# Performance work log

Hardware: AMD Instinct MI355X
Metric: run time of the kernel (lower is better)

Reference implementation:

```python
import jax, jax.numpy as jnp
import numpy as np

IMG_SIZE = 416
NUM_CLASSES = 80
IGNORE_THR = 0.5
EPS = 1e-12
# raw YOLOv3 anchors per feature map, scaled by that level's stride (32,16,8)
ANCHORS = np.array([[[116,90],[156,198],[373,326]],
                    [[30,61],[62,45],[59,119]],
                    [[10,13],[16,30],[33,23]]], dtype=np.float32)
SCALED_ANCHORS = ANCHORS / np.array([32.0,16.0,8.0], dtype=np.float32)[:,None,None]  # [M=3,K=3,2]


def _get_target(targets, total_anchors, fsizes, last_num):
    # Vectorized translation of YOLO3Loss.get_target (including its 3*gi*gj indexing scheme).
    B, N, _ = targets.shape
    A = total_anchors
    sa = jnp.asarray(SCALED_ANCHORS)
    M, K, _ = SCALED_ANCHORS.shape
    fs = jnp.asarray(fsizes, dtype=targets.dtype)        # [M]
    ln = jnp.asarray(last_num, dtype=jnp.int32)          # [M] anchor offsets per level

    valid = jnp.sum(targets, axis=-1) != 0               # [B,N] skip all-zero rows
    cls_idx = targets[..., 0].astype(jnp.int32)          # int(target[b,n,0])
    gx = targets[..., 1:2] * fs                          # [B,N,M]
    gy = targets[..., 2:3] * fs
    gw = targets[..., 3:4] * fs
    gh = targets[..., 4:5] * fs
    gi = jnp.floor(gx).astype(jnp.int32)
    gj = jnp.floor(gy).astype(jnp.int32)

    # IoU of (0,0,gw,gh) gt boxes vs (0,0,aw,ah) anchor shapes -> [B,N,M,K]
    aw, ah = sa[..., 0], sa[..., 1]                      # [M,K]
    inter = jnp.minimum(gw[..., None], aw) * jnp.minimum(gh[..., None], ah)
    union = gw[..., None] * gh[..., None] + aw * ah - inter
    iou = inter / (union + 1e-16)

    # noobj_mask: zero every anchor whose IoU exceeds the ignore threshold
    cell = ln + K * gi * gj                              # [B,N,M]  (last_num[m] + 3*gi*gj)
    idx_no = cell[..., None] + jnp.arange(K)             # [B,N,M,K]
    hit = valid[..., None, None] & (iou > IGNORE_THR)
    safe_no = jnp.where(hit, idx_no, A)                  # route inactive scatters to dummy slot A
    bb = jnp.arange(B)[:, None, None, None]
    noobj = jnp.ones((B, A + 1), targets.dtype).at[bb, safe_no].set(0.0)[:, :A]

    # best anchor over all feature maps
    best_iou_m = jnp.max(iou, -1)                        # [B,N,M]
    best_a_m = jnp.argmax(iou, -1)
    bf = jnp.argmax(best_iou_m, -1)                      # [B,N] best feature map
    take = lambda arr: jnp.take_along_axis(arr, bf[..., None], axis=-1)[..., 0]
    best_a = take(best_a_m)
    gi_b, gj_b = take(gi), take(gj)
    idx_best = ln[bf] + K * gi_b * gj_b + best_a         # [B,N]
    tconf_v = jnp.max(best_iou_m, -1)

    safe = jnp.where(valid, idx_best, A)
    b2 = jnp.arange(B)[:, None]
    def scat(vals):
        return jnp.zeros((B, A + 1), targets.dtype).at[b2, safe].set(vals)[:, :A]
    mask = scat(jnp.ones_like(tconf_v))
    tx = scat(targets[..., 1] * IMG_SIZE)
    ty = scat(targets[..., 2] * IMG_SIZE)
    tw = scat(targets[..., 3] * IMG_SIZE)
    th = scat(targets[..., 4] * IMG_SIZE)
    wwh = scat(2.0 - targets[..., 3] * targets[..., 4])
    tconf = scat(tconf_v)
    tcls = jnp.zeros((B, A + 1, NUM_CLASSES), targets.dtype).at[b2, safe, cls_idx].set(1.0)[:, :A]
    return mask, noobj, tx, ty, tw, th, wwh, tconf, tcls


def _bce(p, t):
    p = jnp.clip(p, EPS, 1.0 - EPS)
    return jnp.mean(-(t * jnp.log(p) + (1.0 - t) * jnp.log(1.0 - p)))


def yolo_loss(prediction, targets, stride):
    B, A, _ = prediction.shape
    M, K, _ = SCALED_ANCHORS.shape
    fsizes = [int(IMG_SIZE / stride * (2 ** i)) for i in range(M)]
    last_num = [0]
    for i in range(M - 1):
        last_num.append(last_num[i] + K * fsizes[i] ** 2)
    mask, noobj, tx, ty, tw, th, wwh, tconf, tcls = _get_target(targets, A, fsizes, last_num)

    x, y = prediction[..., 0], prediction[..., 1]
    w, h = prediction[..., 2], prediction[..., 3]
    conf = prediction[..., 4]
    pcls = prediction[..., 5:]

    mse = lambda a, b: jnp.mean((a - b) ** 2)
    loss_x = mse(x * mask * wwh, tx * wwh)
    loss_y = mse(y * mask * wwh, ty * wwh)
    loss_w = mse(w * mask * wwh, tw * wwh)
    loss_h = mse(h * mask * wwh, th * wwh)
    loss_conf = _bce(conf * mask, tconf) + 0.5 * _bce(conf * noobj, jnp.zeros_like(conf))

    # BCE over boolean-indexed positive rows == mask-weighted mean over all rows
    p = jnp.clip(pcls, EPS, 1.0 - EPS)
    elem = -(tcls * jnp.log(p) + (1.0 - tcls) * jnp.log(1.0 - p))
    npos = jnp.sum(mask)
    loss_cls = jnp.sum(elem * mask[..., None]) / (npos * NUM_CLASSES)
    return loss_x + loss_y + loss_w + loss_h + loss_conf + loss_cls


def setup_inputs() -> dict:
    key = jax.random.key(0)
    k1, k2, k3, k4 = jax.random.split(key, 4)
    B, N, A, C = 64, 50, 10647, NUM_CLASSES
    cls = jax.random.randint(k1, (B, N, 1), 0, C).astype(jnp.float32)
    xy = jax.random.uniform(k2, (B, N, 2), minval=0.05, maxval=0.95)
    wh = jax.random.uniform(k3, (B, N, 2), minval=0.02, maxval=0.4)
    targets = jnp.concatenate([cls, xy, wh], axis=-1)
    # last 10 target slots per image are padding (all zeros -> skipped)
    targets = targets * (jnp.arange(N) < 40).astype(jnp.float32)[None, :, None]
    prediction = jax.random.uniform(k4, (B, A, 5 + C), minval=1e-4, maxval=1.0 - 1e-4)
    return {"prediction": prediction, "targets": targets, "stride": 32}


def reference(prediction, targets, stride):
    return yolo_loss(prediction, targets, stride)
```

## Files before the change

kernel.cpp:

```cpp
#include <hip/hip_runtime.h>
#include <math.h>

#define A_TOT   10647
#define BATCH   64
#define NTGT    50
#define NC      80
#define MAXREC  64
#define MAXHIT  512
#define TOT_CELLS (BATCH * A_TOT)
#define NB4     666
#define CHUNK   1024

struct Rec {
    int cell;
    float tx, ty, tw, th, wwh, tconf;
    unsigned c0, c1, c2;
};

__global__ __launch_bounds__(64) void phaseA(const float* __restrict__ tgt,
                                             int* __restrict__ counts,
                                             Rec* __restrict__ recs,
                                             int* __restrict__ hitcnt,
                                             int* __restrict__ hitlist,
                                             double* __restrict__ sums) {
    __shared__ int   s_valid[64];
    __shared__ int   s_idx[64];
    __shared__ float s_tx[64], s_ty[64], s_tw[64], s_th[64], s_wwh[64], s_tc[64];
    __shared__ int   s_cls[64];
    __shared__ Rec   s_rec[NTGT];
    __shared__ int   s_cnt;
    __shared__ unsigned s_bm[336];
    __shared__ int   s_hits[MAXHIT];
    __shared__ int   s_hc;

    const int b = blockIdx.x;
    const int n = threadIdx.x;

    if (b == 0 && n == 0) {
        sums[0] = 0.0; sums[1] = 0.0; sums[2] = 0.0;
    }

    for (int i = n; i < 336; i += 64) s_bm[i] = 0u;
    if (n == 0) s_hc = 0;
    __syncthreads();

    const float fs[3] = {13.f, 26.f, 52.f};
    const int   ln[3] = {0, 507, 2535};
    const float aw[3][3] = {{3.625f, 4.875f, 11.65625f},
                            {1.875f, 3.875f, 3.6875f},
                            {1.25f,  2.0f,   4.125f}};
    const float ah[3][3] = {{2.8125f, 6.1875f, 10.1875f},
                            {3.8125f, 2.8125f, 7.4375f},
                            {1.625f,  3.75f,   2.875f}};

    int valid = 0;
    if (n < NTGT) {
        const float* t = tgt + (size_t)(b * NTGT + n) * 5;
        float t0 = t[0], t1 = t[1], t2 = t[2], t3 = t[3], t4 = t[4];
        valid = ((t0 + t1 + t2 + t3 + t4) != 0.0f);
        if (valid) {
            float best_m_iou = -1.f;
            int bf = 0, best_a = 0, gi_b = 0, gj_b = 0;
            for (int m = 0; m < 3; m++) {
                float gw = t3 * fs[m], gh = t4 * fs[m];
                int gi = (int)floorf(t1 * fs[m]);
                int gj = (int)floorf(t2 * fs[m]);
                float bi = -1.f; int bk = 0;
                for (int k = 0; k < 3; k++) {
                    float in_ = fminf(gw, aw[m][k]) * fminf(gh, ah[m][k]);
                    float un  = gw * gh + aw[m][k] * ah[m][k] - in_;
                    float iou = in_ / (un + 1e-16f);
                    if (iou > bi) { bi = iou; bk = k; }
                    if (iou > 0.5f) {
                        int cell = ln[m] + 3 * gi * gj + k;
                        unsigned bit = 1u << (cell & 31);
                        unsigned old = atomicOr(&s_bm[cell >> 5], bit);
                        if (!(old & bit)) {
                            int pos = atomicAdd(&s_hc, 1);
                            s_hits[pos] = cell;
                        }
                    }
                }
                if (bi > best_m_iou) { best_m_iou = bi; bf = m; best_a = bk; gi_b = gi; gj_b = gj; }
            }
            s_idx[n] = ln[bf] + 3 * gi_b * gj_b + best_a;
            s_tx[n]  = t1 * 416.f;
            s_ty[n]  = t2 * 416.f;
            s_tw[n]  = t3 * 416.f;
            s_th[n]  = t4 * 416.f;
            s_wwh[n] = 2.0f - t3 * t4;
            s_tc[n]  = best_m_iou;
            s_cls[n] = (int)t0;
        }
    }
    s_valid[n] = valid;
    __syncthreads();

    if (n == 0) {
        int cnt = 0;
        for (int i = 0; i < NTGT; i++) {
            if (!s_valid[i]) continue;
            int cell = s_idx[i];
            int j = -1;
            for (int q = 0; q < cnt; q++)
                if (s_rec[q].cell == cell) { j = q; break; }
            if (j < 0) {
                j = cnt++;
                s_rec[j].cell = cell;
                s_rec[j].c0 = 0u; s_rec[j].c1 = 0u; s_rec[j].c2 = 0u;
            }
            s_rec[j].tx = s_tx[i];  s_rec[j].ty = s_ty[i];
            s_rec[j].tw = s_tw[i];  s_rec[j].th = s_th[i];
            s_rec[j].wwh = s_wwh[i]; s_rec[j].tconf = s_tc[i];
            int c = s_cls[i];
            if (c < 32)       s_rec[j].c0 |= 1u << c;
            else if (c < 64)  s_rec[j].c1 |= 1u << (c - 32);
            else              s_rec[j].c2 |= 1u << (c - 64);
        }
        s_cnt = cnt;
        counts[b] = cnt;
        hitcnt[b] = s_hc;
    }
    __syncthreads();
    for (int r = n; r < s_cnt; r += 64)
        recs[b * MAXREC + r] = s_rec[r];
    for (int i = n; i < s_hc; i += 64)
        hitlist[b * MAXHIT + i] = s_hits[i];
}

__global__ __launch_bounds__(256) void sumK(const float* __restrict__ pred,
                                            const int* __restrict__ counts,
                                            const Rec* __restrict__ recs,
                                            const int* __restrict__ hitcnt,
                                            const int* __restrict__ hitlist,
                                            double* __restrict__ sums) {
    const int bid = blockIdx.x;
    const int tid = threadIdx.x;

    if (bid < NB4) {
        const int base = bid * CHUNK + tid;
        const int i0 = base, i1 = base + 256, i2 = base + 512, i3 = base + 768;
        float v0 = (i0 < TOT_CELLS) ? pred[(size_t)i0 * 85 + 4] : 0.0f;
        float v1 = (i1 < TOT_CELLS) ? pred[(size_t)i1 * 85 + 4] : 0.0f;
        float v2 = (i2 < TOT_CELLS) ? pred[(size_t)i2 * 85 + 4] : 0.0f;
        float v3 = (i3 < TOT_CELLS) ? pred[(size_t)i3 * 85 + 4] : 0.0f;
        double s = -((double)logf(1.0f - v0) + (double)logf(1.0f - v1) +
                     (double)logf(1.0f - v2) + (double)logf(1.0f - v3));
        for (int off = 32; off; off >>= 1) s += __shfl_down(s, off, 64);
        __shared__ double w_[4];
        int lane = tid & 63, w = tid >> 6;
        if (lane == 0) w_[w] = s;
        __syncthreads();
        if (tid == 0) atomicAdd(&sums[1], w_[0] + w_[1] + w_[2] + w_[3]);
    } else {
        const int b = bid - NB4;
        double s1 = 0.0, sA = 0.0, sC = 0.0;
        const int hc = hitcnt[b];
        for (int i = tid; i < hc; i += 256) {
            int cell = hitlist[b * MAXHIT + i];
            float conf = pred[((size_t)b * A_TOT + cell) * 85 + 4];
            s1 += (double)logf(1.0f - conf);
        }
        const int cnt = counts[b];
        for (int r = tid; r < cnt; r += 256) {
            Rec rec = recs[b * MAXREC + r];
            const float* p = pred + ((size_t)b * A_TOT + rec.cell) * 85;
            float x = p[0], y = p[1], w = p[2], h = p[3], conf = p[4];
            float wwh = rec.wwh;
            float dx = x * wwh - rec.tx * wwh;
            float dy = y * wwh - rec.ty * wwh;
            float dw = w * wwh - rec.tw * wwh;
            float dh = h * wwh - rec.th * wwh;
            sA += (double)(dx * dx) + (double)(dy * dy) +
                  (double)(dw * dw) + (double)(dh * dh);
            float t = rec.tconf;
            sA -= (double)(t * logf(conf) + (1.0f - t) * logf(1.0f - conf));
        }
        for (int q = tid; q < cnt * NC; q += 256) {
            int r = q / NC, c = q - r * NC;
            Rec rec = recs[b * MAXREC + r];
            float pc = pred[((size_t)b * A_TOT + rec.cell) * 85 + 5 + c];
            unsigned bit;
            if (c < 32)       bit = (rec.c0 >> c) & 1u;
            else if (c < 64)  bit = (rec.c1 >> (c - 32)) & 1u;
            else              bit = (rec.c2 >> (c - 64)) & 1u;
            sC -= bit ? (double)logf(pc) : (double)logf(1.0f - pc);
        }
        for (int off = 32; off; off >>= 1) {
            s1 += __shfl_down(s1, off, 64);
            sA += __shfl_down(sA, off, 64);
            sC += __shfl_down(sC, off, 64);
        }
        __shared__ double w1[4], wA[4], wC[4];
        int lane = tid & 63, w = tid >> 6;
        if (lane == 0) { w1[w] = s1; wA[w] = sA; wC[w] = sC; }
        __syncthreads();
        if (tid == 0) {
            double t1 = w1[0] + w1[1] + w1[2] + w1[3];
            double tA = wA[0] + wA[1] + wA[2] + wA[3];
            double tC = wC[0] + wC[1] + wC[2] + wC[3];
            if (t1 != 0.0) atomicAdd(&sums[1], t1);
            if (tA != 0.0) atomicAdd(&sums[0], tA);
            if (tC != 0.0) atomicAdd(&sums[2], tC);
        }
    }
}

__global__ void finalK(const double* __restrict__ sums,
                       const int* __restrict__ counts,
                       float* __restrict__ out) {
    if (threadIdx.x == 0) {
        int npos = 0;
        for (int i = 0; i < BATCH; i++) npos += counts[i];
        double total = (sums[0] + 0.5 * sums[1]) / (double)TOT_CELLS;
        if (npos > 0) total += sums[2] / ((double)npos * (double)NC);
        out[0] = (float)total;
    }
}

extern "C" void kernel_launch(void* const* d_in, const int* in_sizes, int n_in,
                              void* d_out, int out_size, void* d_ws, size_t ws_size,
                              hipStream_t stream) {
    const float* pred = (const float*)d_in[0];
    const float* tgt  = (const float*)d_in[1];

    char* ws = (char*)d_ws;
    double* sums    = (double*)ws;
    int*    counts  = (int*)(ws + 64);
    int*    hitcnt  = (int*)(ws + 320);
    int*    hitlist = (int*)(ws + 576);
    Rec*    recs    = (Rec*)(ws + 576 + 131072);

    phaseA<<<BATCH, 64, 0, stream>>>(tgt, counts, recs, hitcnt, hitlist, sums);
    sumK<<<NB4 + BATCH, 256, 0, stream>>>(pred, counts, recs, hitcnt, hitlist, sums);
    finalK<<<1, 64, 0, stream>>>(sums, counts, (float*)d_out);
}
```

Before: 352.3 us.

## Fuse target-building into the reduction kernel and replace atomics with per-block partials

Folds the per-image target-assignment kernel into the main sum kernel. The first 64 blocks now build the hit list and positive records in shared memory and consume them directly, so the global workspace round-trip and one kernel launch go away. Global double atomics are replaced with per-block partial sums that a 256-thread final kernel reduces. The cost is that the serial dedup loop now runs inside the main kernel's blocks, which may delay those blocks.

```diff
diff --git a/kernel.cpp b/kernel.cpp
--- a/kernel.cpp
+++ b/kernel.cpp
@@ -5,11 +5,10 @@
 #define BATCH   64
 #define NTGT    50
 #define NC      80
-#define MAXREC  64
 #define MAXHIT  512
 #define TOT_CELLS (BATCH * A_TOT)
-#define NB4     666
-#define CHUNK   1024
+#define NBD     666
+#define GRID    (BATCH + NBD)
 
 struct Rec {
     int cell;
@@ -17,153 +16,128 @@
     unsigned c0, c1, c2;
 };
 
-__global__ __launch_bounds__(64) void phaseA(const float* __restrict__ tgt,
-                                             int* __restrict__ counts,
-                                             Rec* __restrict__ recs,
-                                             int* __restrict__ hitcnt,
-                                             int* __restrict__ hitlist,
-                                             double* __restrict__ sums) {
-    __shared__ int   s_valid[64];
-    __shared__ int   s_idx[64];
-    __shared__ float s_tx[64], s_ty[64], s_tw[64], s_th[64], s_wwh[64], s_tc[64];
-    __shared__ int   s_cls[64];
-    __shared__ Rec   s_rec[NTGT];
-    __shared__ int   s_cnt;
-    __shared__ unsigned s_bm[336];
-    __shared__ int   s_hits[MAXHIT];
-    __shared__ int   s_hc;
-
-    const int b = blockIdx.x;
-    const int n = threadIdx.x;
-
-    if (b == 0 && n == 0) {
-        sums[0] = 0.0; sums[1] = 0.0; sums[2] = 0.0;
-    }
-
-    for (int i = n; i < 336; i += 64) s_bm[i] = 0u;
-    if (n == 0) s_hc = 0;
-    __syncthreads();
-
-    const float fs[3] = {13.f, 26.f, 52.f};
-    const int   ln[3] = {0, 507, 2535};
-    const float aw[3][3] = {{3.625f, 4.875f, 11.65625f},
-                            {1.875f, 3.875f, 3.6875f},
-                            {1.25f,  2.0f,   4.125f}};
-    const float ah[3][3] = {{2.8125f, 6.1875f, 10.1875f},
-                            {3.8125f, 2.8125f, 7.4375f},
-                            {1.625f,  3.75f,   2.875f}};
-
-    int valid = 0;
-    if (n < NTGT) {
-        const float* t = tgt + (size_t)(b * NTGT + n) * 5;
-        float t0 = t[0], t1 = t[1], t2 = t[2], t3 = t[3], t4 = t[4];
-        valid = ((t0 + t1 + t2 + t3 + t4) != 0.0f);
-        if (valid) {
-            float best_m_iou = -1.f;
-            int bf = 0, best_a = 0, gi_b = 0, gj_b = 0;
-            for (int m = 0; m < 3; m++) {
-                float gw = t3 * fs[m], gh = t4 * fs[m];
-                int gi = (int)floorf(t1 * fs[m]);
-                int gj = (int)floorf(t2 * fs[m]);
-                float bi = -1.f; int bk = 0;
-                for (int k = 0; k < 3; k++) {
-                    float in_ = fminf(gw, aw[m][k]) * fminf(gh, ah[m][k]);
-                    float un  = gw * gh + aw[m][k] * ah[m][k] - in_;
-                    float iou = in_ / (un + 1e-16f);
-                    if (iou > bi) { bi = iou; bk = k; }
-                    if (iou > 0.5f) {
-                        int cell = ln[m] + 3 * gi * gj + k;
-                        unsigned bit = 1u << (cell & 31);
-                        unsigned old = atomicOr(&s_bm[cell >> 5], bit);
-                        if (!(old & bit)) {
-                            int pos = atomicAdd(&s_hc, 1);
-                            s_hits[pos] = cell;
-                        }
-                    }
-                }
-                if (bi > best_m_iou) { best_m_iou = bi; bf = m; best_a = bk; gi_b = gi; gj_b = gj; }
-            }
-            s_idx[n] = ln[bf] + 3 * gi_b * gj_b + best_a;
-            s_tx[n]  = t1 * 416.f;
-            s_ty[n]  = t2 * 416.f;
-            s_tw[n]  = t3 * 416.f;
-            s_th[n]  = t4 * 416.f;
-            s_wwh[n] = 2.0f - t3 * t4;
-            s_tc[n]  = best_m_iou;
-            s_cls[n] = (int)t0;
-        }
-    }
-    s_valid[n] = valid;
-    __syncthreads();
-
-    if (n == 0) {
-        int cnt = 0;
-        for (int i = 0; i < NTGT; i++) {
-            if (!s_valid[i]) continue;
-            int cell = s_idx[i];
-            int j = -1;
-            for (int q = 0; q < cnt; q++)
-                if (s_rec[q].cell == cell) { j = q; break; }
-            if (j < 0) {
-                j = cnt++;
-                s_rec[j].cell = cell;
-                s_rec[j].c0 = 0u; s_rec[j].c1 = 0u; s_rec[j].c2 = 0u;
-            }
-            s_rec[j].tx = s_tx[i];  s_rec[j].ty = s_ty[i];
-            s_rec[j].tw = s_tw[i];  s_rec[j].th = s_th[i];
-            s_rec[j].wwh = s_wwh[i]; s_rec[j].tconf = s_tc[i];
-            int c = s_cls[i];
-            if (c < 32)       s_rec[j].c0 |= 1u << c;
-            else if (c < 64)  s_rec[j].c1 |= 1u << (c - 32);
-            else              s_rec[j].c2 |= 1u << (c - 64);
-        }
-        s_cnt = cnt;
-        counts[b] = cnt;
-        hitcnt[b] = s_hc;
-    }
-    __syncthreads();
-    for (int r = n; r < s_cnt; r += 64)
-        recs[b * MAXREC + r] = s_rec[r];
-    for (int i = n; i < s_hc; i += 64)
-        hitlist[b * MAXHIT + i] = s_hits[i];
-}
-
 __global__ __launch_bounds__(256) void sumK(const float* __restrict__ pred,
-                                            const int* __restrict__ counts,
-                                            const Rec* __restrict__ recs,
-                                            const int* __restrict__ hitcnt,
-                                            const int* __restrict__ hitlist,
-                                            double* __restrict__ sums) {
+                                            const float* __restrict__ tgt,
+                                            double* __restrict__ part,
+                                            int* __restrict__ counts) {
     const int bid = blockIdx.x;
     const int tid = threadIdx.x;
-
-    if (bid < NB4) {
-        const int base = bid * CHUNK + tid;
+    double s1 = 0.0, sA = 0.0, sC = 0.0;
+
+    if (bid >= BATCH) {
+        const int base = (bid - BATCH) * 1024 + tid;
         const int i0 = base, i1 = base + 256, i2 = base + 512, i3 = base + 768;
         float v0 = (i0 < TOT_CELLS) ? pred[(size_t)i0 * 85 + 4] : 0.0f;
         float v1 = (i1 < TOT_CELLS) ? pred[(size_t)i1 * 85 + 4] : 0.0f;
         float v2 = (i2 < TOT_CELLS) ? pred[(size_t)i2 * 85 + 4] : 0.0f;
         float v3 = (i3 < TOT_CELLS) ? pred[(size_t)i3 * 85 + 4] : 0.0f;
-        double s = -((double)logf(1.0f - v0) + (double)logf(1.0f - v1) +
-                     (double)logf(1.0f - v2) + (double)logf(1.0f - v3));
-        for (int off = 32; off; off >>= 1) s += __shfl_down(s, off, 64);
-        __shared__ double w_[4];
-        int lane = tid & 63, w = tid >> 6;
-        if (lane == 0) w_[w] = s;
+        s1 = -((double)logf(1.0f - v0) + (double)logf(1.0f - v1) +
+               (double)logf(1.0f - v2) + (double)logf(1.0f - v3));
+    } else {
+        const int b = bid;
+        __shared__ int   s_valid[NTGT];
+        __shared__ int   s_idx[NTGT];
+        __shared__ float s_tx[NTGT], s_ty[NTGT], s_tw[NTGT], s_th[NTGT];
+        __shared__ float s_wwh[NTGT], s_tc[NTGT];
+        __shared__ int   s_cls[NTGT];
+        __shared__ Rec   s_rec[NTGT];
+        __shared__ int   s_cnt;
+        __shared__ unsigned s_bm[336];
+        __shared__ int   s_hits[MAXHIT];
+        __shared__ int   s_hc;
+
+        for (int i = tid; i < 336; i += 256) s_bm[i] = 0u;
+        if (tid == 0) s_hc = 0;
         __syncthreads();
-        if (tid == 0) atomicAdd(&sums[1], w_[0] + w_[1] + w_[2] + w_[3]);
-    } else {
-        const int b = bid - NB4;
-        double s1 = 0.0, sA = 0.0, sC = 0.0;
-        const int hc = hitcnt[b];
+
+        const float fs[3] = {13.f, 26.f, 52.f};
+        const int   ln[3] = {0, 507, 2535};
+        const float aw[3][3] = {{3.625f, 4.875f, 11.65625f},
+                                {1.875f, 3.875f, 3.6875f},
+                                {1.25f,  2.0f,   4.125f}};
+        const float ah[3][3] = {{2.8125f, 6.1875f, 10.1875f},
+                                {3.8125f, 2.8125f, 7.4375f},
+                                {1.625f,  3.75f,   2.875f}};
+
+        if (tid < NTGT) {
+            const float* t = tgt + (size_t)(b * NTGT + tid) * 5;
+            float t0 = t[0], t1 = t[1], t2 = t[2], t3 = t[3], t4 = t[4];
+            int valid = ((t0 + t1 + t2 + t3 + t4) != 0.0f);
+            s_valid[tid] = valid;
+            if (valid) {
+                float best_m_iou = -1.f;
+                int bf = 0, best_a = 0, gi_b = 0, gj_b = 0;
+                for (int m = 0; m < 3; m++) {
+                    float gw = t3 * fs[m], gh = t4 * fs[m];
+                    int gi = (int)floorf(t1 * fs[m]);
+                    int gj = (int)floorf(t2 * fs[m]);
+                    float bi = -1.f; int bk = 0;
+                    for (int k = 0; k < 3; k++) {
+                        float in_ = fminf(gw, aw[m][k]) * fminf(gh, ah[m][k]);
+                        float un  = gw * gh + aw[m][k] * ah[m][k] - in_;
+                        float iou = in_ / (un + 1e-16f);
+                        if (iou > bi) { bi = iou; bk = k; }
+                        if (iou > 0.5f) {
+                            int cell = ln[m] + 3 * gi * gj + k;
+                            unsigned bit = 1u << (cell & 31);
+                            unsigned old = atomicOr(&s_bm[cell >> 5], bit);
+                            if (!(old & bit)) {
+                                int pos = atomicAdd(&s_hc, 1);
+                                s_hits[pos] = cell;
+                            }
+                        }
+                    }
+                    if (bi > best_m_iou) {
+                        best_m_iou = bi; bf = m; best_a = bk; gi_b = gi; gj_b = gj;
+                    }
+                }
+                s_idx[tid] = ln[bf] + 3 * gi_b * gj_b + best_a;
+                s_tx[tid]  = t1 * 416.f;
+                s_ty[tid]  = t2 * 416.f;
+                s_tw[tid]  = t3 * 416.f;
+                s_th[tid]  = t4 * 416.f;
+                s_wwh[tid] = 2.0f - t3 * t4;
+                s_tc[tid]  = best_m_iou;
+                s_cls[tid] = (int)t0;
+            }
+        }
+        __syncthreads();
+
+        if (tid == 0) {
+            int cnt = 0;
+            for (int i = 0; i < NTGT; i++) {
+                if (!s_valid[i]) continue;
+                int cell = s_idx[i];
+                int j = -1;
+                for (int q = 0; q < cnt; q++)
+                    if (s_rec[q].cell == cell) { j = q; break; }
+                if (j < 0) {
+                    j = cnt++;
+                    s_rec[j].cell = cell;
+                    s_rec[j].c0 = 0u; s_rec[j].c1 = 0u; s_rec[j].c2 = 0u;
+                }
+                s_rec[j].tx = s_tx[i];  s_rec[j].ty = s_ty[i];
+                s_rec[j].tw = s_tw[i];  s_rec[j].th = s_th[i];
+                s_rec[j].wwh = s_wwh[i]; s_rec[j].tconf = s_tc[i];
+                int c = s_cls[i];
+                if (c < 32)       s_rec[j].c0 |= 1u << c;
+                else if (c < 64)  s_rec[j].c1 |= 1u << (c - 32);
+                else              s_rec[j].c2 |= 1u << (c - 64);
+            }
+            s_cnt = cnt;
+            counts[b] = cnt;
+        }
+        __syncthreads();
+        const int cnt = s_cnt;
+        const int hc  = s_hc;
+
         for (int i = tid; i < hc; i += 256) {
-            int cell = hitlist[b * MAXHIT + i];
+            int cell = s_hits[i];
             float conf = pred[((size_t)b * A_TOT + cell) * 85 + 4];
             s1 += (double)logf(1.0f - conf);
         }
-        const int cnt = counts[b];
         for (int r = tid; r < cnt; r += 256) {
-            Rec rec = recs[b * MAXREC + r];
+            Rec rec = s_rec[r];
             const float* p = pred + ((size_t)b * A_TOT + rec.cell) * 85;
             float x = p[0], y = p[1], w = p[2], h = p[3], conf = p[4];
             float wwh = rec.wwh;
@@ -178,7 +152,7 @@
         }
         for (int q = tid; q < cnt * NC; q += 256) {
             int r = q / NC, c = q - r * NC;
-            Rec rec = recs[b * MAXREC + r];
+            Rec rec = s_rec[r];
             float pc = pred[((size_t)b * A_TOT + rec.cell) * 85 + 5 + c];
             unsigned bit;
             if (c < 32)       bit = (rec.c0 >> c) & 1u;
@@ -186,34 +160,53 @@
             else              bit = (rec.c2 >> (c - 64)) & 1u;
             sC -= bit ? (double)logf(pc) : (double)logf(1.0f - pc);
         }
-        for (int off = 32; off; off >>= 1) {
-            s1 += __shfl_down(s1, off, 64);
-            sA += __shfl_down(sA, off, 64);
-            sC += __shfl_down(sC, off, 64);
-        }
-        __shared__ double w1[4], wA[4], wC[4];
-        int lane = tid & 63, w = tid >> 6;
-        if (lane == 0) { w1[w] = s1; wA[w] = sA; wC[w] = sC; }
-        __syncthreads();
-        if (tid == 0) {
-            double t1 = w1[0] + w1[1] + w1[2] + w1[3];
-            double tA = wA[0] + wA[1] + wA[2] + wA[3];
-            double tC = wC[0] + wC[1] + wC[2] + wC[3];
-            if (t1 != 0.0) atomicAdd(&sums[1], t1);
-            if (tA != 0.0) atomicAdd(&sums[0], tA);
-            if (tC != 0.0) atomicAdd(&sums[2], tC);
-        }
+    }
+
+    for (int off = 32; off; off >>= 1) {
+        s1 += __shfl_down(s1, off, 64);
+        sA += __shfl_down(sA, off, 64);
+        sC += __shfl_down(sC, off, 64);
+    }
+    __shared__ double w1[4], wA[4], wC[4];
+    int lane = tid & 63, w = tid >> 6;
+    if (lane == 0) { w1[w] = s1; wA[w] = sA; wC[w] = sC; }
+    __syncthreads();
+    if (tid == 0) {
+        part[bid * 3 + 0] = w1[0] + w1[1] + w1[2] + w1[3];
+        part[bid * 3 + 1] = wA[0] + wA[1] + wA[2] + wA[3];
+        part[bid * 3 + 2] = wC[0] + wC[1] + wC[2] + wC[3];
     }
 }
 
-__global__ void finalK(const double* __restrict__ sums,
-                       const int* __restrict__ counts,
-                       float* __restrict__ out) {
-    if (threadIdx.x == 0) {
-        int npos = 0;
-        for (int i = 0; i < BATCH; i++) npos += counts[i];
-        double total = (sums[0] + 0.5 * sums[1]) / (double)TOT_CELLS;
-        if (npos > 0) total += sums[2] / ((double)npos * (double)NC);
+__global__ __launch_bounds__(256) void finalK(const double* __restrict__ part,
+                                              const int* __restrict__ counts,
+                                              float* __restrict__ out) {
+    const int tid = threadIdx.x;
+    double s1 = 0.0, sA = 0.0, sC = 0.0;
+    for (int i = tid; i < GRID; i += 256) {
+        s1 += part[i * 3 + 0];
+        sA += part[i * 3 + 1];
+        sC += part[i * 3 + 2];
+    }
+    int np = (tid < BATCH) ? counts[tid] : 0;
+    for (int off = 32; off; off >>= 1) {
+        s1 += __shfl_down(s1, off, 64);
+        sA += __shfl_down(sA, off, 64);
+        sC += __shfl_down(sC, off, 64);
+        np += __shfl_down(np, off, 64);
+    }
+    __shared__ double w1[4], wA[4], wC[4];
+    __shared__ int    wN[4];
+    int lane = tid & 63, w = tid >> 6;
+    if (lane == 0) { w1[w] = s1; wA[w] = sA; wC[w] = sC; wN[w] = np; }
+    __syncthreads();
+    if (tid == 0) {
+        double f1 = w1[0] + w1[1] + w1[2] + w1[3];
+        double fA = wA[0] + wA[1] + wA[2] + wA[3];
+        double fC = wC[0] + wC[1] + wC[2] + wC[3];
+        int npos  = wN[0] + wN[1] + wN[2] + wN[3];
+        double total = (fA + 0.5 * f1) / (double)TOT_CELLS;
+        if (npos > 0) total += fC / ((double)npos * (double)NC);
         out[0] = (float)total;
     }
 }
@@ -225,13 +218,9 @@
     const float* tgt  = (const float*)d_in[1];
 
     char* ws = (char*)d_ws;
-    double* sums    = (double*)ws;
-    int*    counts  = (int*)(ws + 64);
-    int*    hitcnt  = (int*)(ws + 320);
-    int*    hitlist = (int*)(ws + 576);
-    Rec*    recs    = (Rec*)(ws + 576 + 131072);
-
-    phaseA<<<BATCH, 64, 0, stream>>>(tgt, counts, recs, hitcnt, hitlist, sums);
-    sumK<<<NB4 + BATCH, 256, 0, stream>>>(pred, counts, recs, hitcnt, hitlist, sums);
-    finalK<<<1, 64, 0, stream>>>(sums, counts, (float*)d_out);
+    double* part   = (double*)ws;
+    int*    counts = (int*)(ws + 32768);
+
+    sumK<<<GRID, 256, 0, stream>>>(pred, tgt, part, counts);
+    finalK<<<1, 256, 0, stream>>>(part, counts, (float*)d_out);
 }
```

Result: faster. 339.5 us (median of 2 runs) (-3.6%).
